# Kernel optimization log

Hardware: AMD Instinct MI355X
Metric: run time of the kernel (lower is better)

Reference implementation:

```python
import jax, jax.numpy as jnp
import numpy as np

B, N_FEAT, D = 16384, 32, 64
HID1, HID2, HOF = 1024, 512, 64
OUT = 1
N_PAIRS = N_FEAT * (N_FEAT - 1) // 2
EPS = 1e-5


def setup_inputs() -> dict:
    key = jax.random.key(0)
    ks = jax.random.split(key, 16)
    s = 0.02
    return {
        "x": jax.random.normal(ks[0], (B, N_FEAT, D), dtype=jnp.float32),
        "W1": jax.random.normal(ks[1], (N_FEAT * D, HID1), dtype=jnp.float32) * s,
        "b1": jnp.zeros((HID1,), jnp.float32),
        "g1": jnp.ones((HID1,), jnp.float32),
        "beta1": jnp.zeros((HID1,), jnp.float32),
        "W2": jax.random.normal(ks[2], (HID1, HID2), dtype=jnp.float32) * s,
        "b2": jnp.zeros((HID2,), jnp.float32),
        "g2": jnp.ones((HID2,), jnp.float32),
        "beta2": jnp.zeros((HID2,), jnp.float32),
        "W3": jax.random.normal(ks[3], (HID2, HOF), dtype=jnp.float32) * s,
        "b3": jnp.zeros((HOF,), jnp.float32),
        "Wc": jax.random.normal(ks[4], (HOF + N_PAIRS, OUT), dtype=jnp.float32) * s,
        "bc": jnp.zeros((OUT,), jnp.float32),
    }


def _batchnorm(h, g, beta):
    # BatchNorm1d in training mode: batch mean / biased variance
    m = jnp.mean(h, axis=0)
    v = jnp.var(h, axis=0)
    return g * (h - m) * jax.lax.rsqrt(v + EPS) + beta


_IU, _JU = np.triu_indices(N_FEAT, k=1)  # same (i<j) order as nested loop


def reference(x, W1, b1, g1, beta1, W2, b2, g2, beta2, W3, b3, Wc, bc):
    # second-order interactions: all pairwise dot products, gathered upper-tri
    gram = jnp.einsum("bnd,bmd->bnm", x, x)          # [B, N, N]
    pairs = gram[:, _IU, _JU]                          # [B, N*(N-1)/2]
    # deep processor
    flat = x.reshape(x.shape[0], -1)                   # [B, N*D]
    h = _batchnorm(jax.nn.relu(flat @ W1 + b1), g1, beta1)
    h = _batchnorm(jax.nn.relu(h @ W2 + b2), g2, beta2)
    hof = h @ W3 + b3                                  # [B, HOF]
    inter = jnp.concatenate([hof, pairs], axis=1)
    return inter @ Wc + bc
```

## Files before the change

kernel.cpp:

```cpp
#include <hip/hip_runtime.h>
#include <stdint.h>

typedef unsigned short u16;
typedef unsigned char u8;
typedef __attribute__((ext_vector_type(8))) short short8;
typedef __attribute__((ext_vector_type(4))) float f32x4;
typedef __attribute__((ext_vector_type(16))) float f32x16;
typedef __attribute__((ext_vector_type(4))) int i32x4;
typedef __attribute__((ext_vector_type(8))) int i32x8;

#define BATCH 16384L
#define WSCALE 64.0f
#define INV_WSCALE (1.0f / 64.0f)
#define SCALE_ONE 0x7f7f7f7f

__device__ __forceinline__ u16 f2bf(float f) {
    union { float f; uint32_t u; } cv; cv.f = f;
    uint32_t u = cv.u;
    u = (u + 0x7fffu + ((u >> 16) & 1u)) >> 16;
    return (u16)u;
}
__device__ __forceinline__ float bf2f(u16 h) {
    union { uint32_t u; float f; } cv; cv.u = ((uint32_t)h) << 16;
    return cv.f;
}
template<bool HI>
__device__ __forceinline__ uint32_t fp8pk(float a, float b, uint32_t old) {
    return (uint32_t)__builtin_amdgcn_cvt_pk_fp8_f32(a, b, (int)old, HI);
}
__device__ __forceinline__ u8 f2fp8(float v) {
    return (u8)(__builtin_amdgcn_cvt_pk_fp8_f32(v, v, 0, false) & 0xff);
}

__global__ __launch_bounds__(256) void k_gram(const float* __restrict__ x,
                                              const float* __restrict__ Wc,
                                              u8* __restrict__ xb,
                                              float* __restrict__ spair) {
    const int wave = threadIdx.x >> 6;
    const int lane = threadIdx.x & 63;
    const long b = (long)blockIdx.x * 4 + wave;
    const int r16 = lane & 15, quad = lane >> 4;
    const float* xg = x + b * 2048;

    short8 hi[2][2], lo[2][2];
    for (int mt = 0; mt < 2; mt++) {
        for (int k0 = 0; k0 < 2; k0++) {
            const int row = mt * 16 + r16;
            const int kof = k0 * 32 + quad * 8;
            const float* p = xg + row * 64 + kof;
            float4 p0 = *(const float4*)p;
            float4 p1 = *(const float4*)(p + 4);
            float v[8] = {p0.x, p0.y, p0.z, p0.w, p1.x, p1.y, p1.z, p1.w};
            short8 h, l;
            for (int j = 0; j < 8; j++) {
                u16 hb = f2bf(v[j]);
                h[j] = (short)hb;
                l[j] = (short)f2bf(v[j] - bf2f(hb));
            }
            hi[mt][k0] = h; lo[mt][k0] = l;
            uint32_t w0 = fp8pk<false>(v[0], v[1], 0); w0 = fp8pk<true>(v[2], v[3], w0);
            uint32_t w1 = fp8pk<false>(v[4], v[5], 0); w1 = fp8pk<true>(v[6], v[7], w1);
            *(uint2*)(xb + b * 2048 + row * 64 + kof) = make_uint2(w0, w1);
        }
    }
    f32x4 zero = {0.f, 0.f, 0.f, 0.f};
    f32x4 acc[2][2];
    for (int mt = 0; mt < 2; mt++) for (int nt = 0; nt < 2; nt++) acc[mt][nt] = zero;
    for (int k0 = 0; k0 < 2; k0++)
        for (int mt = 0; mt < 2; mt++)
            for (int nt = 0; nt < 2; nt++) {
                acc[mt][nt] = __builtin_amdgcn_mfma_f32_16x16x32_bf16(hi[mt][k0], hi[nt][k0], acc[mt][nt], 0, 0, 0);
                acc[mt][nt] = __builtin_amdgcn_mfma_f32_16x16x32_bf16(hi[mt][k0], lo[nt][k0], acc[mt][nt], 0, 0, 0);
                acc[mt][nt] = __builtin_amdgcn_mfma_f32_16x16x32_bf16(lo[mt][k0], hi[nt][k0], acc[mt][nt], 0, 0, 0);
            }
    float pacc = 0.f;
    for (int mt = 0; mt < 2; mt++)
        for (int nt = 0; nt < 2; nt++)
            for (int r = 0; r < 4; r++) {
                int row = mt * 16 + quad * 4 + r;
                int col = nt * 16 + r16;
                if (col > row) {
                    int p = 31 * row - (row * (row - 1)) / 2 + (col - row - 1);
                    pacc += acc[mt][nt][r] * Wc[64 + p];
                }
            }
    for (int off = 1; off < 64; off <<= 1) pacc += __shfl_xor(pacc, off);
    if (lane == 0) spair[b] = pacc;
}

__global__ __launch_bounds__(256) void k_transpose_fp8(const float* __restrict__ W,
                                                       const float* __restrict__ scale,
                                                       u8* __restrict__ WT,
                                                       int K, int N) {
    __shared__ float tile[32][33];
    const int nb = blockIdx.x * 32, kb = blockIdx.y * 32;
    const int tx = threadIdx.x & 31, ty = threadIdx.x >> 5;
    if (scale) {
        for (int r = ty; r < 32; r += 8)
            tile[r][tx] = scale[kb + r] * W[(long)(kb + r) * N + nb + tx];
    } else {
        for (int r = ty; r < 32; r += 8)
            tile[r][tx] = W[(long)(kb + r) * N + nb + tx];
    }
    __syncthreads();
    for (int r = ty; r < 32; r += 8)
        WT[(long)(nb + r) * K + kb + tx] = f2fp8(WSCALE * tile[tx][r]);
}

__device__ __forceinline__ i32x8 frag32(const u8* __restrict__ lds, int R, int cb) {
    const int s = R & 7;
    i32x4 lo = *(const i32x4*)&lds[R * 128 + ((cb ^ s) * 16)];
    i32x4 hi = *(const i32x4*)&lds[R * 128 + (((cb + 1) ^ s) * 16)];
    i32x8 r;
    r[0] = lo[0]; r[1] = lo[1]; r[2] = lo[2]; r[3] = lo[3];
    r[4] = hi[0]; r[5] = hi[1]; r[6] = hi[2]; r[7] = hi[3];
    return r;
}

template<int LOGNB>
__global__ __launch_bounds__(256) void gemm_bn(const u8* __restrict__ A,
                                               const u8* __restrict__ Bt,
                                               const float* __restrict__ bias,
                                               u8* __restrict__ C,
                                               float* __restrict__ sums,
                                               float* __restrict__ ssq,
                                               int N, int K, float inv) {
    __shared__ u8 lA[128 * 128];
    __shared__ u8 lB[128 * 128];
    const int tid = threadIdx.x;
    const int lane = tid & 63, wave = tid >> 6;
    const int wm = wave >> 1, wn = wave & 1;
    const int r32 = lane & 31, hf = lane >> 5;
    const int lid = blockIdx.x;
    const int xcd = lid & 7, t = lid >> 3;
    const int nbk = t & ((1 << LOGNB) - 1);
    const int mbk = (xcd << 4) + (t >> LOGNB);
    const long m0 = (long)mbk * 128;
    const long n0 = (long)nbk * 128;

    f32x16 acc[2][2];
    for (int mt = 0; mt < 2; mt++)
        for (int nt = 0; nt < 2; nt++)
            for (int r = 0; r < 16; r++) acc[mt][nt][r] = 0.f;

    for (long k0 = 0; k0 < K; k0 += 128) {
        __syncthreads();
        for (int i = 0; i < 4; i++) {
            const int c = tid + 256 * i;
            const int row = c >> 3, pos = c & 7;
            const int g = pos ^ (row & 7);
            const u8* ga = A + (m0 + row) * K + k0 + g * 16;
            const u8* gb = Bt + (n0 + row) * K + k0 + g * 16;
            __builtin_amdgcn_global_load_lds((const __attribute__((address_space(1))) void*)ga,
                                             (__attribute__((address_space(3))) void*)(&lA[c * 16]), 16, 0, 0);
            __builtin_amdgcn_global_load_lds((const __attribute__((address_space(1))) void*)gb,
                                             (__attribute__((address_space(3))) void*)(&lB[c * 16]), 16, 0, 0);
        }
        __syncthreads();
        for (int km = 0; km < 2; km++) {
            const int cb = km * 4 + hf * 2;
            i32x8 af[2], bfr[2];
            for (int mt = 0; mt < 2; mt++)
                af[mt] = frag32(lA, wm * 64 + mt * 32 + r32, cb);
            for (int nt = 0; nt < 2; nt++)
                bfr[nt] = frag32(lB, wn * 64 + nt * 32 + r32, cb);
            for (int mt = 0; mt < 2; mt++)
                for (int nt = 0; nt < 2; nt++)
                    acc[mt][nt] = __builtin_amdgcn_mfma_scale_f32_32x32x64_f8f6f4(
                        af[mt], bfr[nt], acc[mt][nt], 0, 0,
                        0, SCALE_ONE, 0, SCALE_ONE);
        }
    }

    for (int nt = 0; nt < 2; nt++) {
        const int col = (int)n0 + wn * 64 + nt * 32 + r32;
        const float bcol = bias[col];
        float s = 0.f, sq = 0.f;
        for (int mt = 0; mt < 2; mt++)
            for (int r = 0; r < 16; r++) {
                const long row = m0 + wm * 64 + mt * 32 + 4 * hf + (r & 3) + 8 * (r >> 2);
                float v = acc[mt][nt][r] * inv + bcol;
                v = fmaxf(v, 0.f);
                C[row * N + col] = f2fp8(v);
                s += v; sq += v * v;
            }
        s += __shfl_xor(s, 32);
        sq += __shfl_xor(sq, 32);
        if (hf == 0) { atomicAdd(&sums[col], s); atomicAdd(&ssq[col], sq); }
    }
}

__global__ void k_stat(const float* __restrict__ sums, const float* __restrict__ ssq,
                       const float* __restrict__ g, const float* __restrict__ beta,
                       float* __restrict__ a, float* __restrict__ c, int n, float invB) {
    const int k = blockIdx.x * 256 + threadIdx.x;
    if (k < n) {
        const float m = sums[k] * invB;
        const float var = ssq[k] * invB - m * m;
        const float s = g[k] * rsqrtf(var + 1e-5f);
        a[k] = s; c[k] = beta[k] - s * m;
    }
}

__global__ void k_stat2v(const float* __restrict__ sums, const float* __restrict__ ssq,
                         const float* __restrict__ g, const float* __restrict__ beta,
                         float* __restrict__ a, float* __restrict__ c, float invB,
                         const float* __restrict__ W3, const float* __restrict__ b3,
                         const float* __restrict__ Wc, const float* __restrict__ bc,
                         float* __restrict__ v, float* __restrict__ c0) {
    if (blockIdx.x < 2) {
        const int k = blockIdx.x * 256 + threadIdx.x;
        const float m = sums[k] * invB;
        const float var = ssq[k] * invB - m * m;
        const float s = g[k] * rsqrtf(var + 1e-5f);
        a[k] = s; c[k] = beta[k] - s * m;
    } else {
        for (int k = threadIdx.x; k < 512; k += 256) {
            float s = 0.f;
            for (int j = 0; j < 64; j++) s += W3[k * 64 + j] * Wc[j];
            v[k] = s;
        }
        if (threadIdx.x == 0) {
            float s = 0.f;
            for (int j = 0; j < 64; j++) s += b3[j] * Wc[j];
            *c0 = s + bc[0];
        }
    }
}

__global__ __launch_bounds__(64) void k_b2adj(const float* __restrict__ W2,
                                              const float* __restrict__ c1,
                                              const float* __restrict__ b2,
                                              float* __restrict__ b2a) {
    const int col = blockIdx.x, lane = threadIdx.x;
    float s = 0.f;
    for (int k = lane; k < 1024; k += 64) s += c1[k] * W2[(long)k * 512 + col];
    for (int off = 1; off < 64; off <<= 1) s += __shfl_xor(s, off);
    if (lane == 0) b2a[col] = b2[col] + s;
}

__global__ __launch_bounds__(256) void k_final(const u8* __restrict__ h2,
                                               const float* __restrict__ a2,
                                               const float* __restrict__ c2,
                                               const float* __restrict__ v,
                                               const float* __restrict__ c0,
                                               const float* __restrict__ spair,
                                               float* __restrict__ out) {
    const int wave = threadIdx.x >> 6, lane = threadIdx.x & 63;
    const long b = (long)blockIdx.x * 4 + wave;
    const int k0 = lane * 8;
    uint2 hv = *(const uint2*)&h2[b * 512 + k0];
    float f[8];
    f[0] = __builtin_amdgcn_cvt_f32_fp8(hv.x, 0);
    f[1] = __builtin_amdgcn_cvt_f32_fp8(hv.x, 1);
    f[2] = __builtin_amdgcn_cvt_f32_fp8(hv.x, 2);
    f[3] = __builtin_amdgcn_cvt_f32_fp8(hv.x, 3);
    f[4] = __builtin_amdgcn_cvt_f32_fp8(hv.y, 0);
    f[5] = __builtin_amdgcn_cvt_f32_fp8(hv.y, 1);
    f[6] = __builtin_amdgcn_cvt_f32_fp8(hv.y, 2);
    f[7] = __builtin_amdgcn_cvt_f32_fp8(hv.y, 3);
    float acc = 0.f;
    for (int j = 0; j < 8; j++) {
        const int k = k0 + j;
        acc += (a2[k] * f[j] + c2[k]) * v[k];
    }
    for (int off = 1; off < 64; off <<= 1) acc += __shfl_xor(acc, off);
    if (lane == 0) out[b] = acc + spair[b] + c0[0];
}

extern "C" void kernel_launch(void* const* d_in, const int* in_sizes, int n_in,
                              void* d_out, int out_size, void* d_ws, size_t ws_size,
                              hipStream_t stream) {
    const float* x     = (const float*)d_in[0];
    const float* W1    = (const float*)d_in[1];
    const float* b1    = (const float*)d_in[2];
    const float* g1    = (const float*)d_in[3];
    const float* beta1 = (const float*)d_in[4];
    const float* W2    = (const float*)d_in[5];
    const float* b2    = (const float*)d_in[6];
    const float* g2    = (const float*)d_in[7];
    const float* beta2 = (const float*)d_in[8];
    const float* W3    = (const float*)d_in[9];
    const float* b3    = (const float*)d_in[10];
    const float* Wc    = (const float*)d_in[11];
    const float* bc    = (const float*)d_in[12];
    float* out = (float*)d_out;

    char* ws = (char*)d_ws;
    size_t o = 0;
    u8* xb  = (u8*)(ws + o); o += BATCH * 2048;
    u8* w1f = (u8*)(ws + o); o += 2048L * 1024;
    u8* w2f = (u8*)(ws + o); o += 1024L * 512;
    u8* h1b = (u8*)(ws + o); o += BATCH * 1024;
    u8* h2b = (u8*)(ws + o); o += BATCH * 512;
    float* spair = (float*)(ws + o); o += BATCH * 4;
    float* stats = (float*)(ws + o); o += 3072 * 4;
    float* sums1 = stats, *ssq1 = stats + 1024, *sums2 = stats + 2048, *ssq2 = stats + 2560;
    float* a1 = (float*)(ws + o); o += 1024 * 4;
    float* c1 = (float*)(ws + o); o += 1024 * 4;
    float* a2 = (float*)(ws + o); o += 512 * 4;
    float* c2 = (float*)(ws + o); o += 512 * 4;
    float* vv = (float*)(ws + o); o += 512 * 4;
    float* c0 = (float*)(ws + o); o += 4;
    float* b2a = (float*)(ws + o); o += 512 * 4;

    (void)hipMemsetAsync(stats, 0, 3072 * 4, stream);
    k_gram<<<4096, 256, 0, stream>>>(x, Wc, xb, spair);
    k_transpose_fp8<<<dim3(1024 / 32, 2048 / 32), 256, 0, stream>>>(W1, nullptr, w1f, 2048, 1024);
    gemm_bn<3><<<1024, 256, 0, stream>>>(xb, w1f, b1, h1b, sums1, ssq1, 1024, 2048, INV_WSCALE);
    k_stat<<<4, 256, 0, stream>>>(sums1, ssq1, g1, beta1, a1, c1, 1024, 1.f / 16384.f);
    k_transpose_fp8<<<dim3(512 / 32, 1024 / 32), 256, 0, stream>>>(W2, a1, w2f, 1024, 512);
    k_b2adj<<<512, 64, 0, stream>>>(W2, c1, b2, b2a);
    gemm_bn<2><<<512, 256, 0, stream>>>(h1b, w2f, b2a, h2b, sums2, ssq2, 512, 1024, INV_WSCALE);
    k_stat2v<<<3, 256, 0, stream>>>(sums2, ssq2, g2, beta2, a2, c2, 1.f / 16384.f,
                                    W3, b3, Wc, bc, vv, c0);
    k_final<<<4096, 256, 0, stream>>>(h2b, a2, c2, vv, c0, spair, out);
}
```

Measured before the change: 318.1 us.

## Double-buffer GEMM LDS tiles, truncate bf16 split, and remap b2 bias kernel

The fp8 GEMM now keeps two LDS buffers per operand and issues the next K-tile's global-to-LDS loads before computing on the current tile, so memory latency can overlap with the MFMA work. A single barrier per iteration is kept. The gram kernel's hi/lo bf16 split uses truncation instead of round-to-nearest, which cuts ALU work while the lo term still carries the residual. The b2 adjustment kernel changes from one wave per column with a shuffle reduction to one thread per column with a serial loop, launched as 8 blocks. Double buffering doubles LDS use to 64KB, which may lower occupancy, and the reworked bias kernel has much less parallelism.

```diff
diff --git a/kernel.cpp b/kernel.cpp
--- a/kernel.cpp
+++ b/kernel.cpp
@@ -19,6 +19,10 @@
     uint32_t u = cv.u;
     u = (u + 0x7fffu + ((u >> 16) & 1u)) >> 16;
     return (u16)u;
+}
+__device__ __forceinline__ u16 f2bf_trunc(float f) {
+    union { float f; uint32_t u; } cv; cv.f = f;
+    return (u16)(cv.u >> 16);
 }
 __device__ __forceinline__ float bf2f(u16 h) {
     union { uint32_t u; float f; } cv; cv.u = ((uint32_t)h) << 16;
@@ -53,9 +57,9 @@
             float v[8] = {p0.x, p0.y, p0.z, p0.w, p1.x, p1.y, p1.z, p1.w};
             short8 h, l;
             for (int j = 0; j < 8; j++) {
-                u16 hb = f2bf(v[j]);
+                u16 hb = f2bf_trunc(v[j]);
                 h[j] = (short)hb;
-                l[j] = (short)f2bf(v[j] - bf2f(hb));
+                l[j] = (short)f2bf_trunc(v[j] - bf2f(hb));
             }
             hi[mt][k0] = h; lo[mt][k0] = l;
             uint32_t w0 = fp8pk<false>(v[0], v[1], 0); w0 = fp8pk<true>(v[2], v[3], w0);
@@ -125,8 +129,8 @@
                                                float* __restrict__ sums,
                                                float* __restrict__ ssq,
                                                int N, int K, float inv) {
-    __shared__ u8 lA[128 * 128];
-    __shared__ u8 lB[128 * 128];
+    __shared__ u8 lA[2][128 * 128];
+    __shared__ u8 lB[2][128 * 128];
     const int tid = threadIdx.x;
     const int lane = tid & 63, wave = tid >> 6;
     const int wm = wave >> 1, wn = wave & 1;
@@ -143,8 +147,9 @@
         for (int nt = 0; nt < 2; nt++)
             for (int r = 0; r < 16; r++) acc[mt][nt][r] = 0.f;
 
-    for (long k0 = 0; k0 < K; k0 += 128) {
-        __syncthreads();
+    const int nit = K >> 7;
+
+    auto stage = [&](int buf, long k0) {
         for (int i = 0; i < 4; i++) {
             const int c = tid + 256 * i;
             const int row = c >> 3, pos = c & 7;
@@ -152,18 +157,24 @@
             const u8* ga = A + (m0 + row) * K + k0 + g * 16;
             const u8* gb = Bt + (n0 + row) * K + k0 + g * 16;
             __builtin_amdgcn_global_load_lds((const __attribute__((address_space(1))) void*)ga,
-                                             (__attribute__((address_space(3))) void*)(&lA[c * 16]), 16, 0, 0);
+                                             (__attribute__((address_space(3))) void*)(&lA[buf][c * 16]), 16, 0, 0);
             __builtin_amdgcn_global_load_lds((const __attribute__((address_space(1))) void*)gb,
-                                             (__attribute__((address_space(3))) void*)(&lB[c * 16]), 16, 0, 0);
-        }
+                                             (__attribute__((address_space(3))) void*)(&lB[buf][c * 16]), 16, 0, 0);
+        }
+    };
+
+    stage(0, 0);
+    for (int it = 0; it < nit; it++) {
+        const int cur = it & 1;
         __syncthreads();
+        if (it + 1 < nit) stage(cur ^ 1, (long)(it + 1) << 7);
         for (int km = 0; km < 2; km++) {
             const int cb = km * 4 + hf * 2;
             i32x8 af[2], bfr[2];
             for (int mt = 0; mt < 2; mt++)
-                af[mt] = frag32(lA, wm * 64 + mt * 32 + r32, cb);
+                af[mt] = frag32(lA[cur], wm * 64 + mt * 32 + r32, cb);
             for (int nt = 0; nt < 2; nt++)
-                bfr[nt] = frag32(lB, wn * 64 + nt * 32 + r32, cb);
+                bfr[nt] = frag32(lB[cur], wn * 64 + nt * 32 + r32, cb);
             for (int mt = 0; mt < 2; mt++)
                 for (int nt = 0; nt < 2; nt++)
                     acc[mt][nt] = __builtin_amdgcn_mfma_scale_f32_32x32x64_f8f6f4(
@@ -232,11 +243,10 @@
                                               const float* __restrict__ c1,
                                               const float* __restrict__ b2,
                                               float* __restrict__ b2a) {
-    const int col = blockIdx.x, lane = threadIdx.x;
+    const int col = blockIdx.x * 64 + threadIdx.x;
     float s = 0.f;
-    for (int k = lane; k < 1024; k += 64) s += c1[k] * W2[(long)k * 512 + col];
-    for (int off = 1; off < 64; off <<= 1) s += __shfl_xor(s, off);
-    if (lane == 0) b2a[col] = b2[col] + s;
+    for (int k = 0; k < 1024; k++) s += c1[k] * W2[(long)k * 512 + col];
+    b2a[col] = b2[col] + s;
 }
 
 __global__ __launch_bounds__(256) void k_final(const u8* __restrict__ h2,
@@ -310,7 +320,7 @@
     gemm_bn<3><<<1024, 256, 0, stream>>>(xb, w1f, b1, h1b, sums1, ssq1, 1024, 2048, INV_WSCALE);
     k_stat<<<4, 256, 0, stream>>>(sums1, ssq1, g1, beta1, a1, c1, 1024, 1.f / 16384.f);
     k_transpose_fp8<<<dim3(512 / 32, 1024 / 32), 256, 0, stream>>>(W2, a1, w2f, 1024, 512);
-    k_b2adj<<<512, 64, 0, stream>>>(W2, c1, b2, b2a);
+    k_b2adj<<<8, 64, 0, stream>>>(W2, c1, b2, b2a);
     gemm_bn<2><<<512, 256, 0, stream>>>(h1b, w2f, b2a, h2b, sums2, ssq2, 512, 1024, INV_WSCALE);
     k_stat2v<<<3, 256, 0, stream>>>(sums2, ssq2, g2, beta2, a2, c2, 1.f / 16384.f,
                                     W3, b3, Wc, bc, vv, c0);
```

After: 334.4 us. 5.1% more time.
